# Kernel optimization log

Hardware: AMD Instinct MI355X
Metric: run time of the kernel (lower is better)

The kernel has to match this reference:

```python
import jax, jax.numpy as jnp
import numpy as np

N = 100000   # local subgraph nodes
E = 600000   # directed edges
D = 128      # memory_dim
B = 10000    # label nodes queried
C = 32       # num_classes


def _glorot(key, shape):
    s = 1.0 / np.sqrt(shape[0])
    return jax.random.uniform(key, shape, jnp.float32, -s, s)


def setup_inputs() -> dict:
    key = jax.random.key(0)
    ks = jax.random.split(key, 16)
    return {
        "node_state": jax.random.normal(ks[0], (N, D), jnp.float32),
        "edge_index": jax.random.randint(ks[1], (2, E), 0, N),
        "label_pos": jax.random.randint(ks[2], (B,), 0, N),
        # SAGEConv 1: lin_l (neighbor, with bias), lin_r (root, no bias)
        "W1l": _glorot(ks[3], (D, D)), "b1l": jnp.zeros((D,), jnp.float32),
        "W1r": _glorot(ks[4], (D, D)),
        # SAGEConv 2
        "W2l": _glorot(ks[5], (D, D)), "b2l": jnp.zeros((D,), jnp.float32),
        "W2r": _glorot(ks[6], (D, D)),
        # classifier: Linear(D,D) -> ReLU -> Linear(D,C)
        "Wc1": _glorot(ks[7], (D, D)), "bc1": jnp.zeros((D,), jnp.float32),
        "Wc2": _glorot(ks[8], (D, C)), "bc2": jnp.zeros((C,), jnp.float32),
    }


def _sage(x, src, dst, Wl, bl, Wr):
    # PyG SAGEConv, aggr='mean': out_i = lin_l(mean_{j: (j->i)} x_j) + lin_r(x_i)
    n = x.shape[0]
    agg = jax.ops.segment_sum(x[src], dst, num_segments=n)          # [N, D]
    cnt = jax.ops.segment_sum(jnp.ones_like(dst, x.dtype), dst, num_segments=n)
    mean = agg / jnp.maximum(cnt, 1.0)[:, None]
    return mean @ Wl + bl + x @ Wr


def reference(node_state, edge_index, label_pos,
              W1l, b1l, W1r, W2l, b2l, W2r, Wc1, bc1, Wc2, bc2):
    src, dst = edge_index[0], edge_index[1]
    x = jax.nn.relu(_sage(node_state, src, dst, W1l, b1l, W1r))
    x = jax.nn.relu(_sage(x, src, dst, W2l, b2l, W2r))
    h = jax.nn.relu(x[label_pos] @ Wc1 + bc1)                        # [B, D]
    return h @ Wc2 + bc2                                             # [B, C]
```

## Files before the change

### kernel.cpp

```cpp
#include <hip/hip_runtime.h>
#include <hip/hip_bf16.h>

static constexpr int N = 100000;
static constexpr int E = 600000;
static constexpr int D = 128;
static constexpr int B = 10000;
static constexpr int C = 32;
static constexpr int NB = (N + 1023) / 1024;
static constexpr int TOUCHB = (N * (D / 4) + 255) / 256;

typedef __attribute__((ext_vector_type(8))) short short8;
typedef __attribute__((ext_vector_type(4))) float f32x4;

static __device__ __forceinline__ unsigned short f2bf(float f) {
    unsigned u = __float_as_uint(f);
    unsigned r = (u + 0x7FFFu + ((u >> 16) & 1u)) >> 16;
    return (unsigned short)r;
}
static __device__ __forceinline__ float bf2f(unsigned short h) {
    return __uint_as_float(((unsigned)h) << 16);
}

static __device__ __forceinline__ void split8(const float4 v0, const float4 v1,
                                              short8& h, short8& l) {
    const float f[8] = {v0.x, v0.y, v0.z, v0.w, v1.x, v1.y, v1.z, v1.w};
    #pragma unroll
    for (int i = 0; i < 8; ++i) {
        unsigned short hh = f2bf(f[i]);
        h[i] = (short)hh;
        l[i] = (short)f2bf(f[i] - bf2f(hh));
    }
}

__global__ void lab_k(const int* __restrict__ label_pos, int* __restrict__ labflag,
                      int* __restrict__ flag, int nlab) {
    int i = blockIdx.x * blockDim.x + threadIdx.x;
    if (i < nlab) {
        int v = label_pos[i];
        labflag[v] = 1;
        flag[v] = 1;
    }
}

__global__ __launch_bounds__(256) void deg_swz_k(
    const int* __restrict__ src, const int* __restrict__ dst,
    const int* __restrict__ labflag,
    int* __restrict__ deg, int* __restrict__ flag, int nE, int EB,
    const float* W0, const float* W1, const float* W2, const float* W3,
    const float* W4, const float* W5,
    unsigned short* __restrict__ out,
    const float* __restrict__ xtouch, float* __restrict__ sink) {
    if ((int)blockIdx.x < EB) {
        int e = blockIdx.x * 256 + threadIdx.x;
        if (e < nE) {
            int d = dst[e];
            atomicAdd(&deg[d], 1);
            if (labflag[d]) flag[src[e]] = 1;
        }
        return;
    }
    if ((int)blockIdx.x < EB + 80) {
        const int sb = blockIdx.x - EB;
        const int m = sb >> 4;
        const int chunk = sb & 15;
        const float* W = (m == 0) ? W0 : (m == 1) ? W1 : (m == 2) ? W2
                       : (m == 3) ? W3 : W4;
        unsigned short* o = out + (size_t)m * 32768;
        #pragma unroll
        for (int it = 0; it < 4; ++it) {
            int f = chunk * 1024 + it * 256 + threadIdx.x;
            int j = f & 7;
            int lane = (f >> 3) & 63;
            int fi = f >> 9;
            int k = (fi >> 3) * 32 + (lane >> 4) * 8 + j;
            int n = (fi & 7) * 16 + (lane & 15);
            float a = W[k * 128 + n];
            unsigned short h = f2bf(a);
            o[f] = h;
            o[16384 + f] = f2bf(a - bf2f(h));
        }
        return;
    }
    if ((int)blockIdx.x == EB + 80) {
        unsigned short* o2 = out + (size_t)5 * 32768;
        #pragma unroll
        for (int it = 0; it < 16; ++it) {
            int f = it * 256 + threadIdx.x;
            int j = f & 7;
            int lane = (f >> 3) & 63;
            int fi = f >> 9;
            int k = (fi >> 1) * 32 + (lane >> 4) * 8 + j;
            int n = (fi & 1) * 16 + (lane & 15);
            float a = W5[k * 32 + n];
            unsigned short h = f2bf(a);
            o2[f] = h;
            o2[4096 + f] = f2bf(a - bf2f(h));
        }
        return;
    }
    const int f4 = (blockIdx.x - (EB + 81)) * 256 + threadIdx.x;
    if (f4 < N * (D / 4)) {
        float4 v = reinterpret_cast<const float4*>(xtouch)[f4];
        float s = v.x + v.y + v.z + v.w;
        if (s > 1e30f) *sink = s;
    }
}

__global__ __launch_bounds__(256) void scan1m_k(const int* __restrict__ deg,
                                                const int* __restrict__ flag,
                                                int* __restrict__ bsum, int n) {
    __shared__ int lsum[256];
    const int t = threadIdx.x;
    const bool isdeg = (int)blockIdx.x < NB;
    const int bloc = isdeg ? blockIdx.x : blockIdx.x - NB;
    const int* v = isdeg ? deg : flag;
    const int base = bloc * 1024 + t * 4;
    int s = 0;
    #pragma unroll
    for (int i = 0; i < 4; ++i) {
        int idx = base + i;
        if (idx < n) s += v[idx];
    }
    lsum[t] = s;
    __syncthreads();
    for (int off = 128; off > 0; off >>= 1) {
        if (t < off) lsum[t] += lsum[t + off];
        __syncthreads();
    }
    if (t == 0) bsum[blockIdx.x] = lsum[0];
}

__global__ __launch_bounds__(256) void scan3m_k(
    const int* __restrict__ deg, const int* __restrict__ flag,
    const int* __restrict__ bsum,
    int* __restrict__ roff, int* __restrict__ cur,
    int* __restrict__ map, int* __restrict__ ulist, int* __restrict__ ucnt,
    int n)
{
    __shared__ int sb[128];
    __shared__ int lsum[256];
    const int t = threadIdx.x;
    const bool isdeg = (int)blockIdx.x < NB;
    const int bloc = isdeg ? blockIdx.x : blockIdx.x - NB;
    const int* bs = isdeg ? bsum : bsum + NB;
    const int* v  = isdeg ? deg : flag;

    if (t < 128) sb[t] = (t < NB) ? bs[t] : 0;
    __syncthreads();
    for (int off = 1; off < 128; off <<= 1) {
        int u = (t < 128 && t >= off) ? sb[t - off] : 0;
        __syncthreads();
        if (t < 128) sb[t] += u;
        __syncthreads();
    }
    const int boff = (bloc == 0) ? 0 : sb[bloc - 1];
    if (bloc == 0 && t == 0) {
        if (isdeg) roff[n] = sb[NB - 1];
        else *ucnt = sb[NB - 1];
    }

    const int base = bloc * 1024 + t * 4;
    int d[4];
    int s = 0;
    #pragma unroll
    for (int i = 0; i < 4; ++i) {
        int idx = base + i;
        d[i] = (idx < n) ? v[idx] : 0;
        s += d[i];
    }
    lsum[t] = s;
    __syncthreads();
    for (int off = 1; off < 256; off <<= 1) {
        int u = (t >= off) ? lsum[t - off] : 0;
        __syncthreads();
        lsum[t] += u;
        __syncthreads();
    }
    int run = boff + lsum[t] - s;
    #pragma unroll
    for (int i = 0; i < 4; ++i) {
        int idx = base + i;
        if (idx < n) {
            if (isdeg) {
                roff[idx] = run;
                cur[idx]  = run;
                run += d[i];
            } else if (d[i]) {
                map[idx] = run;
                ulist[run] = idx;
                ++run;
            }
        }
    }
}

__global__ void fill_k(const int* __restrict__ src, const int* __restrict__ dst,
                       int* __restrict__ cur, int* __restrict__ csr_src, int nE) {
    int e = blockIdx.x * blockDim.x + threadIdx.x;
    if (e < nE) {
        int p = atomicAdd(&cur[dst[e]], 1);
        csr_src[p] = src[e];
    }
}

template <bool GATHER, bool MAP>
__global__ __launch_bounds__(256) void gather_mean_k(
    const float* __restrict__ x, const int* __restrict__ roff,
    const int* __restrict__ csr_src, const int* __restrict__ rows,
    const int* __restrict__ map, const int* __restrict__ nrows_ptr,
    float* __restrict__ out, int nrows_max) {
    const int nrows = nrows_ptr ? nrows_ptr[0] : nrows_max;
    const int w = blockIdx.x * (blockDim.x >> 6) + (threadIdx.x >> 6);
    if (w >= nrows) return;
    const int lane = threadIdx.x & 63;
    const int n  = GATHER ? rows[w] : w;
    const int jb = roff[n];
    const int je = roff[n + 1];
    const float* xb = x + lane * 2;

    float ax = 0.f, ay = 0.f;
    int j = jb;
    for (; j + 4 <= je; j += 4) {
        int s0 = csr_src[j + 0];
        int s1 = csr_src[j + 1];
        int s2 = csr_src[j + 2];
        int s3 = csr_src[j + 3];
        if (MAP) { s0 = map[s0]; s1 = map[s1]; s2 = map[s2]; s3 = map[s3]; }
        float2 v0 = *reinterpret_cast<const float2*>(xb + (size_t)s0 * D);
        float2 v1 = *reinterpret_cast<const float2*>(xb + (size_t)s1 * D);
        float2 v2 = *reinterpret_cast<const float2*>(xb + (size_t)s2 * D);
        float2 v3 = *reinterpret_cast<const float2*>(xb + (size_t)s3 * D);
        ax += v0.x + v1.x + v2.x + v3.x;
        ay += v0.y + v1.y + v2.y + v3.y;
    }
    for (; j < je; ++j) {
        int s = csr_src[j];
        if (MAP) s = map[s];
        float2 v = *reinterpret_cast<const float2*>(xb + (size_t)s * D);
        ax += v.x;
        ay += v.y;
    }
    const float inv = 1.0f / fmaxf((float)(je - jb), 1.0f);
    *reinterpret_cast<float2*>(out + (size_t)w * D + lane * 2) =
        make_float2(ax * inv, ay * inv);
}

template <bool GATHER, bool MAP>
__global__ __launch_bounds__(256, 6) void sage_mfma_k(
    const float* __restrict__ mean, const float* __restrict__ xsrc,
    const int* __restrict__ rows, const int* __restrict__ map,
    const int* __restrict__ nrows_ptr,
    const unsigned short* __restrict__ WlSw, const unsigned short* __restrict__ WrSw,
    const float* __restrict__ bl, float* __restrict__ xout, int nrows_max)
{
    const int nrows = nrows_ptr ? nrows_ptr[0] : nrows_max;
    const int rb = blockIdx.x * 32;
    if (rb >= nrows) return;

    const int t = threadIdx.x;
    const int wrow = (t >> 6) & 1;
    const int wcol = t >> 7;
    const int lane = t & 63;
    const int mcol = lane & 15;
    const int q = lane >> 4;
    const int r = rb + wrow * 16 + mcol;

    f32x4 acc[4];
    #pragma unroll
    for (int no = 0; no < 4; ++no) acc[no] = (f32x4){0.f, 0.f, 0.f, 0.f};

    size_t gidx = 0;
    if (r < nrows) {
        int g = GATHER ? rows[r] : r;
        if (MAP) g = map[g];
        gidx = (size_t)g;
    }

    #pragma unroll
    for (int br = 0; br < 2; ++br) {
        const unsigned short* __restrict__ Wm = br ? WrSw : WlSw;
        #pragma unroll
        for (int kp = 0; kp < 4; ++kp) {
            short8 aH, aL;
            {
                float4 v0 = make_float4(0.f, 0.f, 0.f, 0.f);
                float4 v1 = make_float4(0.f, 0.f, 0.f, 0.f);
                if (r < nrows) {
                    const float* p = (br == 0)
                        ? mean + (size_t)r * D + kp * 32 + q * 8
                        : xsrc + gidx * D + kp * 32 + q * 8;
                    v0 = *reinterpret_cast<const float4*>(p);
                    v1 = *reinterpret_cast<const float4*>(p + 4);
                }
                split8(v0, v1, aH, aL);
            }
            #pragma unroll
            for (int no = 0; no < 4; ++no) {
                const size_t fo = ((size_t)(kp * 8 + wcol * 4 + no) * 64 + lane) * 8;
                short8 bh = *reinterpret_cast<const short8*>(Wm + fo);
                short8 bo = *reinterpret_cast<const short8*>(Wm + 16384 + fo);
                acc[no] = __builtin_amdgcn_mfma_f32_16x16x32_bf16(aH, bh, acc[no], 0, 0, 0);
                acc[no] = __builtin_amdgcn_mfma_f32_16x16x32_bf16(aL, bh, acc[no], 0, 0, 0);
                acc[no] = __builtin_amdgcn_mfma_f32_16x16x32_bf16(aH, bo, acc[no], 0, 0, 0);
            }
        }
    }

    #pragma unroll
    for (int no = 0; no < 4; ++no) {
        const int col = wcol * 64 + no * 16 + mcol;
        const float bias = bl[col];
        #pragma unroll
        for (int ri = 0; ri < 4; ++ri) {
            const int row = rb + wrow * 16 + q * 4 + ri;
            if (row < nrows)
                xout[(size_t)row * D + col] = fmaxf(acc[no][ri] + bias, 0.f);
        }
    }
}

__global__ __launch_bounds__(256) void sage2_cls_k(
    const float* __restrict__ mean, const float* __restrict__ x1c,
    const int* __restrict__ label_pos, const int* __restrict__ map,
    const unsigned short* __restrict__ WlSw, const unsigned short* __restrict__ WrSw,
    const float* __restrict__ bl,
    const unsigned short* __restrict__ Wc1Sw, const float* __restrict__ bc1,
    const unsigned short* __restrict__ Wc2Sw, const float* __restrict__ bc2,
    float* __restrict__ out, int nrows)
{
    __shared__ alignas(16) float Xs[32][132];
    __shared__ alignas(16) float Hs[32][132];
    const int rb = blockIdx.x * 32;
    const int t = threadIdx.x;
    const int wrow = (t >> 6) & 1;
    const int wcol = t >> 7;
    const int lane = t & 63;
    const int mcol = lane & 15;
    const int q = lane >> 4;
    const int r = rb + wrow * 16 + mcol;

    f32x4 acc[4];
    #pragma unroll
    for (int no = 0; no < 4; ++no) acc[no] = (f32x4){0.f, 0.f, 0.f, 0.f};

    size_t gidx = 0;
    if (r < nrows) gidx = (size_t)map[label_pos[r]];

    #pragma unroll
    for (int br = 0; br < 2; ++br) {
        const unsigned short* __restrict__ Wm = br ? WrSw : WlSw;
        #pragma unroll
        for (int kp = 0; kp < 4; ++kp) {
            short8 aH, aL;
            {
                float4 v0 = make_float4(0.f, 0.f, 0.f, 0.f);
                float4 v1 = make_float4(0.f, 0.f, 0.f, 0.f);
                if (r < nrows) {
                    const float* p = (br == 0)
                        ? mean + (size_t)r * D + kp * 32 + q * 8
                        : x1c + gidx * D + kp * 32 + q * 8;
                    v0 = *reinterpret_cast<const float4*>(p);
                    v1 = *reinterpret_cast<const float4*>(p + 4);
                }
                split8(v0, v1, aH, aL);
            }
            #pragma unroll
            for (int no = 0; no < 4; ++no) {
                const size_t fo = ((size_t)(kp * 8 + wcol * 4 + no) * 64 + lane) * 8;
                short8 bh = *reinterpret_cast<const short8*>(Wm + fo);
                short8 bo = *reinterpret_cast<const short8*>(Wm + 16384 + fo);
                acc[no] = __builtin_amdgcn_mfma_f32_16x16x32_bf16(aH, bh, acc[no], 0, 0, 0);
                acc[no] = __builtin_amdgcn_mfma_f32_16x16x32_bf16(aL, bh, acc[no], 0, 0, 0);
                acc[no] = __builtin_amdgcn_mfma_f32_16x16x32_bf16(aH, bo, acc[no], 0, 0, 0);
            }
        }
    }

    #pragma unroll
    for (int no = 0; no < 4; ++no) {
        const int col = wcol * 64 + no * 16 + mcol;
        const float bias = bl[col];
        #pragma unroll
        for (int ri = 0; ri < 4; ++ri) {
            const int lrow = wrow * 16 + q * 4 + ri;
            Xs[lrow][col] = fmaxf(acc[no][ri] + bias, 0.f);
        }
    }
    __syncthreads();

    {
        f32x4 acc2[4];
        #pragma unroll
        for (int no = 0; no < 4; ++no) acc2[no] = (f32x4){0.f, 0.f, 0.f, 0.f};

        #pragma unroll
        for (int kp = 0; kp < 4; ++kp) {
            short8 aH, aL;
            {
                const float* p = &Xs[wrow * 16 + mcol][kp * 32 + q * 8];
                float4 v0 = *reinterpret_cast<const float4*>(p);
                float4 v1 = *reinterpret_cast<const float4*>(p + 4);
                split8(v0, v1, aH, aL);
            }
            #pragma unroll
            for (int no = 0; no < 4; ++no) {
                const size_t fo = ((size_t)(kp * 8 + wcol * 4 + no) * 64 + lane) * 8;
                short8 bh = *reinterpret_cast<const short8*>(Wc1Sw + fo);
                short8 bo = *reinterpret_cast<const short8*>(Wc1Sw + 16384 + fo);
                acc2[no] = __builtin_amdgcn_mfma_f32_16x16x32_bf16(aH, bh, acc2[no], 0, 0, 0);
                acc2[no] = __builtin_amdgcn_mfma_f32_16x16x32_bf16(aL, bh, acc2[no], 0, 0, 0);
                acc2[no] = __builtin_amdgcn_mfma_f32_16x16x32_bf16(aH, bo, acc2[no], 0, 0, 0);
            }
        }
        #pragma unroll
        for (int no = 0; no < 4; ++no) {
            const int col = wcol * 64 + no * 16 + mcol;
            const float bias = bc1[col];
            #pragma unroll
            for (int ri = 0; ri < 4; ++ri) {
                const int lrow = wrow * 16 + q * 4 + ri;
                Hs[lrow][col] = fmaxf(acc2[no][ri] + bias, 0.0f);
            }
        }
    }
    __syncthreads();

    {
        f32x4 acc3 = (f32x4){0.f, 0.f, 0.f, 0.f};
        #pragma unroll
        for (int kp = 0; kp < 4; ++kp) {
            short8 aH, aL;
            {
                const float* p = &Hs[wrow * 16 + mcol][kp * 32 + q * 8];
                float4 v0 = *reinterpret_cast<const float4*>(p);
                float4 v1 = *reinterpret_cast<const float4*>(p + 4);
                split8(v0, v1, aH, aL);
            }
            const size_t fo = ((size_t)(kp * 2 + wcol) * 64 + lane) * 8;
            short8 bh = *reinterpret_cast<const short8*>(Wc2Sw + fo);
            short8 bo = *reinterpret_cast<const short8*>(Wc2Sw + 4096 + fo);
            acc3 = __builtin_amdgcn_mfma_f32_16x16x32_bf16(aH, bh, acc3, 0, 0, 0);
            acc3 = __builtin_amdgcn_mfma_f32_16x16x32_bf16(aL, bh, acc3, 0, 0, 0);
            acc3 = __builtin_amdgcn_mfma_f32_16x16x32_bf16(aH, bo, acc3, 0, 0, 0);
        }
        const int col = wcol * 16 + mcol;
        const float b2 = bc2[col];
        #pragma unroll
        for (int ri = 0; ri < 4; ++ri) {
            const int row = rb + wrow * 16 + q * 4 + ri;
            if (row < nrows) out[(size_t)row * C + col] = acc3[ri] + b2;
        }
    }
}


extern "C" void kernel_launch(void* const* d_in, const int* in_sizes, int n_in,
                              void* d_out, int out_size, void* d_ws, size_t ws_size,
                              hipStream_t stream) {
    const float* node_state = (const float*)d_in[0];
    const int*   edge_index = (const int*)d_in[1];
    const int*   label_pos  = (const int*)d_in[2];
    const float* W1l = (const float*)d_in[3];
    const float* b1l = (const float*)d_in[4];
    const float* W1r = (const float*)d_in[5];
    const float* W2l = (const float*)d_in[6];
    const float* b2l = (const float*)d_in[7];
    const float* W2r = (const float*)d_in[8];
    const float* Wc1 = (const float*)d_in[9];
    const float* bc1 = (const float*)d_in[10];
    const float* Wc2 = (const float*)d_in[11];
    const float* bc2 = (const float*)d_in[12];
    float* out = (float*)d_out;

    const int* src = edge_index;
    const int* dst = edge_index + E;

    char* ws = (char*)d_ws;
    float* x1c   = (float*)ws;                    ws += sizeof(float) * (size_t)N * D;
    float* bufA  = (float*)ws;                    ws += sizeof(float) * (size_t)N * D;
    unsigned short* Wsw = (unsigned short*)ws;    ws += sizeof(unsigned short) * (5 * 32768 + 8192);
    int* deg     = (int*)ws;                      ws += sizeof(int) * N;
    int* flag    = (int*)ws;                      ws += sizeof(int) * N;
    int* labflag = (int*)ws;                      ws += sizeof(int) * N;
    int* ucnt    = (int*)ws;                      ws += sizeof(int);
    float* sink  = (float*)ws;                    ws += sizeof(float);
    ws += sizeof(int) * 2;
    int* roff    = (int*)ws;                      ws += sizeof(int) * (N + 1);
    int* cur     = (int*)ws;                      ws += sizeof(int) * N;
    int* csr_src = (int*)ws;                      ws += sizeof(int) * E;
    int* map     = (int*)ws;                      ws += sizeof(int) * N;
    int* ulist   = (int*)ws;                      ws += sizeof(int) * N;
    int* bsum    = (int*)ws;                      ws += sizeof(int) * 256;
    float* mean1c = bufA;
    float* mean2g = bufA;

    const int TB = 256;
    const int EB = (E + TB - 1) / TB;

    hipMemsetAsync(deg, 0, sizeof(int) * (3 * N + 1), stream);
    lab_k<<<(B + TB - 1) / TB, TB, 0, stream>>>(label_pos, labflag, flag, B);
    deg_swz_k<<<EB + 81 + TOUCHB, TB, 0, stream>>>(src, dst, labflag, deg, flag, E, EB,
                                                   W1l, W1r, W2l, W2r, Wc1, Wc2, Wsw,
                                                   node_state, sink);
    scan1m_k<<<2 * NB, 256, 0, stream>>>(deg, flag, bsum, N);
    scan3m_k<<<2 * NB, 256, 0, stream>>>(deg, flag, bsum, roff, cur, map, ulist, ucnt, N);
    fill_k<<<EB, TB, 0, stream>>>(src, dst, cur, csr_src, E);

    gather_mean_k<true, false><<<(N + 3) / 4, TB, 0, stream>>>(
        node_state, roff, csr_src, ulist, nullptr, ucnt, mean1c, N);
    sage_mfma_k<true, false><<<(N + 31) / 32, TB, 0, stream>>>(
        mean1c, node_state, ulist, nullptr, ucnt,
        Wsw, Wsw + 32768, b1l, x1c, N);

    gather_mean_k<true, true><<<(B + 3) / 4, TB, 0, stream>>>(
        x1c, roff, csr_src, label_pos, map, nullptr, mean2g, B);
    sage2_cls_k<<<(B + 31) / 32, TB, 0, stream>>>(
        mean2g, x1c, label_pos, map,
        Wsw + 65536, Wsw + 98304, b2l,
        Wsw + 131072, bc1,
        Wsw + 163840, bc2, out, B);
}
```

Measured before the change: 255.1 us.

## Fuse neighbor mean-gather into SAGE MFMA kernels and replace scans with atomic allocation

```diff
diff --git a/kernel.cpp b/kernel.cpp
--- a/kernel.cpp
+++ b/kernel.cpp
@@ -6,7 +6,6 @@
 static constexpr int D = 128;
 static constexpr int B = 10000;
 static constexpr int C = 32;
-static constexpr int NB = (N + 1023) / 1024;
 static constexpr int TOUCHB = (N * (D / 4) + 255) / 256;
 
 typedef __attribute__((ext_vector_type(8))) short short8;
@@ -106,161 +105,89 @@
     }
 }
 
-__global__ __launch_bounds__(256) void scan1m_k(const int* __restrict__ deg,
-                                                const int* __restrict__ flag,
-                                                int* __restrict__ bsum, int n) {
-    __shared__ int lsum[256];
-    const int t = threadIdx.x;
-    const bool isdeg = (int)blockIdx.x < NB;
-    const int bloc = isdeg ? blockIdx.x : blockIdx.x - NB;
-    const int* v = isdeg ? deg : flag;
-    const int base = bloc * 1024 + t * 4;
-    int s = 0;
-    #pragma unroll
-    for (int i = 0; i < 4; ++i) {
-        int idx = base + i;
-        if (idx < n) s += v[idx];
-    }
-    lsum[t] = s;
-    __syncthreads();
-    for (int off = 128; off > 0; off >>= 1) {
-        if (t < off) lsum[t] += lsum[t + off];
-        __syncthreads();
-    }
-    if (t == 0) bsum[blockIdx.x] = lsum[0];
-}
-
-__global__ __launch_bounds__(256) void scan3m_k(
+__global__ __launch_bounds__(256) void alloc_k(
     const int* __restrict__ deg, const int* __restrict__ flag,
-    const int* __restrict__ bsum,
     int* __restrict__ roff, int* __restrict__ cur,
-    int* __restrict__ map, int* __restrict__ ulist, int* __restrict__ ucnt,
-    int n)
+    int* __restrict__ map, int* __restrict__ ulist,
+    int* __restrict__ ucnt, int* __restrict__ total, int n)
 {
-    __shared__ int sb[128];
-    __shared__ int lsum[256];
-    const int t = threadIdx.x;
-    const bool isdeg = (int)blockIdx.x < NB;
-    const int bloc = isdeg ? blockIdx.x : blockIdx.x - NB;
-    const int* bs = isdeg ? bsum : bsum + NB;
-    const int* v  = isdeg ? deg : flag;
-
-    if (t < 128) sb[t] = (t < NB) ? bs[t] : 0;
-    __syncthreads();
-    for (int off = 1; off < 128; off <<= 1) {
-        int u = (t < 128 && t >= off) ? sb[t - off] : 0;
-        __syncthreads();
-        if (t < 128) sb[t] += u;
-        __syncthreads();
-    }
-    const int boff = (bloc == 0) ? 0 : sb[bloc - 1];
-    if (bloc == 0 && t == 0) {
-        if (isdeg) roff[n] = sb[NB - 1];
-        else *ucnt = sb[NB - 1];
-    }
-
-    const int base = bloc * 1024 + t * 4;
-    int d[4];
-    int s = 0;
-    #pragma unroll
-    for (int i = 0; i < 4; ++i) {
-        int idx = base + i;
-        d[i] = (idx < n) ? v[idx] : 0;
-        s += d[i];
-    }
-    lsum[t] = s;
-    __syncthreads();
-    for (int off = 1; off < 256; off <<= 1) {
-        int u = (t >= off) ? lsum[t - off] : 0;
-        __syncthreads();
-        lsum[t] += u;
-        __syncthreads();
-    }
-    int run = boff + lsum[t] - s;
-    #pragma unroll
-    for (int i = 0; i < 4; ++i) {
-        int idx = base + i;
-        if (idx < n) {
-            if (isdeg) {
-                roff[idx] = run;
-                cur[idx]  = run;
-                run += d[i];
-            } else if (d[i]) {
-                map[idx] = run;
-                ulist[run] = idx;
-                ++run;
-            }
-        }
+    int i = blockIdx.x * 256 + threadIdx.x;
+    if (i < n && flag[i]) {
+        int m = atomicAdd(ucnt, 1);
+        map[i] = m;
+        ulist[m] = i;
+        int d = deg[i];
+        int p = atomicAdd(total, d);
+        roff[i] = p;
+        cur[i] = p;
     }
 }
 
 __global__ void fill_k(const int* __restrict__ src, const int* __restrict__ dst,
+                       const int* __restrict__ flag,
                        int* __restrict__ cur, int* __restrict__ csr_src, int nE) {
     int e = blockIdx.x * blockDim.x + threadIdx.x;
     if (e < nE) {
-        int p = atomicAdd(&cur[dst[e]], 1);
-        csr_src[p] = src[e];
-    }
-}
-
-template <bool GATHER, bool MAP>
-__global__ __launch_bounds__(256) void gather_mean_k(
+        int d = dst[e];
+        if (flag[d]) {
+            int p = atomicAdd(&cur[d], 1);
+            csr_src[p] = src[e];
+        }
+    }
+}
+
+__global__ __launch_bounds__(256, 6) void sage1_fused_k(
     const float* __restrict__ x, const int* __restrict__ roff,
-    const int* __restrict__ csr_src, const int* __restrict__ rows,
-    const int* __restrict__ map, const int* __restrict__ nrows_ptr,
-    float* __restrict__ out, int nrows_max) {
-    const int nrows = nrows_ptr ? nrows_ptr[0] : nrows_max;
-    const int w = blockIdx.x * (blockDim.x >> 6) + (threadIdx.x >> 6);
-    if (w >= nrows) return;
-    const int lane = threadIdx.x & 63;
-    const int n  = GATHER ? rows[w] : w;
-    const int jb = roff[n];
-    const int je = roff[n + 1];
-    const float* xb = x + lane * 2;
-
-    float ax = 0.f, ay = 0.f;
-    int j = jb;
-    for (; j + 4 <= je; j += 4) {
-        int s0 = csr_src[j + 0];
-        int s1 = csr_src[j + 1];
-        int s2 = csr_src[j + 2];
-        int s3 = csr_src[j + 3];
-        if (MAP) { s0 = map[s0]; s1 = map[s1]; s2 = map[s2]; s3 = map[s3]; }
-        float2 v0 = *reinterpret_cast<const float2*>(xb + (size_t)s0 * D);
-        float2 v1 = *reinterpret_cast<const float2*>(xb + (size_t)s1 * D);
-        float2 v2 = *reinterpret_cast<const float2*>(xb + (size_t)s2 * D);
-        float2 v3 = *reinterpret_cast<const float2*>(xb + (size_t)s3 * D);
-        ax += v0.x + v1.x + v2.x + v3.x;
-        ay += v0.y + v1.y + v2.y + v3.y;
-    }
-    for (; j < je; ++j) {
-        int s = csr_src[j];
-        if (MAP) s = map[s];
-        float2 v = *reinterpret_cast<const float2*>(xb + (size_t)s * D);
-        ax += v.x;
-        ay += v.y;
-    }
-    const float inv = 1.0f / fmaxf((float)(je - jb), 1.0f);
-    *reinterpret_cast<float2*>(out + (size_t)w * D + lane * 2) =
-        make_float2(ax * inv, ay * inv);
-}
-
-template <bool GATHER, bool MAP>
-__global__ __launch_bounds__(256, 6) void sage_mfma_k(
-    const float* __restrict__ mean, const float* __restrict__ xsrc,
-    const int* __restrict__ rows, const int* __restrict__ map,
-    const int* __restrict__ nrows_ptr,
+    const int* __restrict__ deg, const int* __restrict__ csr_src,
+    const int* __restrict__ ulist, const int* __restrict__ nrows_ptr,
     const unsigned short* __restrict__ WlSw, const unsigned short* __restrict__ WrSw,
-    const float* __restrict__ bl, float* __restrict__ xout, int nrows_max)
+    const float* __restrict__ bl, float* __restrict__ xout)
 {
-    const int nrows = nrows_ptr ? nrows_ptr[0] : nrows_max;
+    __shared__ alignas(16) float Ms[32][132];
+    const int nrows = nrows_ptr[0];
     const int rb = blockIdx.x * 32;
     if (rb >= nrows) return;
 
     const int t = threadIdx.x;
-    const int wrow = (t >> 6) & 1;
-    const int wcol = t >> 7;
     const int lane = t & 63;
+    const int w = t >> 6;
+
+    {
+        const float* xb = x + lane * 2;
+        for (int lr8 = 0; lr8 < 8; ++lr8) {
+            const int lr = w * 8 + lr8;
+            const int r = rb + lr;
+            int jb = 0, je = 0;
+            if (r < nrows) { const int n = ulist[r]; jb = roff[n]; je = jb + deg[n]; }
+            float ax = 0.f, ay = 0.f;
+            int j = jb;
+            for (; j + 4 <= je; j += 4) {
+                const int s0 = csr_src[j + 0];
+                const int s1 = csr_src[j + 1];
+                const int s2 = csr_src[j + 2];
+                const int s3 = csr_src[j + 3];
+                float2 v0 = *reinterpret_cast<const float2*>(xb + (size_t)s0 * D);
+                float2 v1 = *reinterpret_cast<const float2*>(xb + (size_t)s1 * D);
+                float2 v2 = *reinterpret_cast<const float2*>(xb + (size_t)s2 * D);
+                float2 v3 = *reinterpret_cast<const float2*>(xb + (size_t)s3 * D);
+                ax += v0.x + v1.x + v2.x + v3.x;
+                ay += v0.y + v1.y + v2.y + v3.y;
+            }
+            for (; j < je; ++j) {
+                const int s = csr_src[j];
+                float2 v = *reinterpret_cast<const float2*>(xb + (size_t)s * D);
+                ax += v.x;
+                ay += v.y;
+            }
+            const float inv = 1.0f / fmaxf((float)(je - jb), 1.0f);
+            Ms[lr][lane * 2]     = ax * inv;
+            Ms[lr][lane * 2 + 1] = ay * inv;
+        }
+    }
+    __syncthreads();
+
+    const int wrow = w & 1;
+    const int wcol = w >> 1;
     const int mcol = lane & 15;
     const int q = lane >> 4;
     const int r = rb + wrow * 16 + mcol;
@@ -270,11 +197,7 @@
     for (int no = 0; no < 4; ++no) acc[no] = (f32x4){0.f, 0.f, 0.f, 0.f};
 
     size_t gidx = 0;
-    if (r < nrows) {
-        int g = GATHER ? rows[r] : r;
-        if (MAP) g = map[g];
-        gidx = (size_t)g;
-    }
+    if (r < nrows) gidx = (size_t)ulist[r];
 
     #pragma unroll
     for (int br = 0; br < 2; ++br) {
@@ -283,14 +206,19 @@
         for (int kp = 0; kp < 4; ++kp) {
             short8 aH, aL;
             {
-                float4 v0 = make_float4(0.f, 0.f, 0.f, 0.f);
-                float4 v1 = make_float4(0.f, 0.f, 0.f, 0.f);
-                if (r < nrows) {
-                    const float* p = (br == 0)
-                        ? mean + (size_t)r * D + kp * 32 + q * 8
-                        : xsrc + gidx * D + kp * 32 + q * 8;
+                float4 v0, v1;
+                if (br == 0) {
+                    const float* p = &Ms[wrow * 16 + mcol][kp * 32 + q * 8];
                     v0 = *reinterpret_cast<const float4*>(p);
                     v1 = *reinterpret_cast<const float4*>(p + 4);
+                } else {
+                    v0 = make_float4(0.f, 0.f, 0.f, 0.f);
+                    v1 = make_float4(0.f, 0.f, 0.f, 0.f);
+                    if (r < nrows) {
+                        const float* p = x + gidx * D + kp * 32 + q * 8;
+                        v0 = *reinterpret_cast<const float4*>(p);
+                        v1 = *reinterpret_cast<const float4*>(p + 4);
+                    }
                 }
                 split8(v0, v1, aH, aL);
             }
@@ -319,8 +247,9 @@
     }
 }
 
-__global__ __launch_bounds__(256) void sage2_cls_k(
-    const float* __restrict__ mean, const float* __restrict__ x1c,
+__global__ __launch_bounds__(256) void sage2_cls_fused_k(
+    const float* __restrict__ x1c, const int* __restrict__ roff,
+    const int* __restrict__ deg, const int* __restrict__ csr_src,
     const int* __restrict__ label_pos, const int* __restrict__ map,
     const unsigned short* __restrict__ WlSw, const unsigned short* __restrict__ WrSw,
     const float* __restrict__ bl,
@@ -328,13 +257,50 @@
     const unsigned short* __restrict__ Wc2Sw, const float* __restrict__ bc2,
     float* __restrict__ out, int nrows)
 {
+    __shared__ alignas(16) float Ms[32][132];
     __shared__ alignas(16) float Xs[32][132];
     __shared__ alignas(16) float Hs[32][132];
     const int rb = blockIdx.x * 32;
     const int t = threadIdx.x;
-    const int wrow = (t >> 6) & 1;
-    const int wcol = t >> 7;
     const int lane = t & 63;
+    const int w = t >> 6;
+
+    {
+        const float* xb = x1c + lane * 2;
+        for (int lr8 = 0; lr8 < 8; ++lr8) {
+            const int lr = w * 8 + lr8;
+            const int r = rb + lr;
+            int jb = 0, je = 0;
+            if (r < nrows) { const int n = label_pos[r]; jb = roff[n]; je = jb + deg[n]; }
+            float ax = 0.f, ay = 0.f;
+            int j = jb;
+            for (; j + 4 <= je; j += 4) {
+                const int s0 = map[csr_src[j + 0]];
+                const int s1 = map[csr_src[j + 1]];
+                const int s2 = map[csr_src[j + 2]];
+                const int s3 = map[csr_src[j + 3]];
+                float2 v0 = *reinterpret_cast<const float2*>(xb + (size_t)s0 * D);
+                float2 v1 = *reinterpret_cast<const float2*>(xb + (size_t)s1 * D);
+                float2 v2 = *reinterpret_cast<const float2*>(xb + (size_t)s2 * D);
+                float2 v3 = *reinterpret_cast<const float2*>(xb + (size_t)s3 * D);
+                ax += v0.x + v1.x + v2.x + v3.x;
+                ay += v0.y + v1.y + v2.y + v3.y;
+            }
+            for (; j < je; ++j) {
+                const int s = map[csr_src[j]];
+                float2 v = *reinterpret_cast<const float2*>(xb + (size_t)s * D);
+                ax += v.x;
+                ay += v.y;
+            }
+            const float inv = 1.0f / fmaxf((float)(je - jb), 1.0f);
+            Ms[lr][lane * 2]     = ax * inv;
+            Ms[lr][lane * 2 + 1] = ay * inv;
+        }
+    }
+    __syncthreads();
+
+    const int wrow = w & 1;
+    const int wcol = w >> 1;
     const int mcol = lane & 15;
     const int q = lane >> 4;
     const int r = rb + wrow * 16 + mcol;
@@ -353,14 +319,19 @@
         for (int kp = 0; kp < 4; ++kp) {
             short8 aH, aL;
             {
-                float4 v0 = make_float4(0.f, 0.f, 0.f, 0.f);
-                float4 v1 = make_float4(0.f, 0.f, 0.f, 0.f);
-                if (r < nrows) {
-                    const float* p = (br == 0)
-                        ? mean + (size_t)r * D + kp * 32 + q * 8
-                        : x1c + gidx * D + kp * 32 + q * 8;
+                float4 v0, v1;
+                if (br == 0) {
+                    const float* p = &Ms[wrow * 16 + mcol][kp * 32 + q * 8];
                     v0 = *reinterpret_cast<const float4*>(p);
                     v1 = *reinterpret_cast<const float4*>(p + 4);
+                } else {
+                    v0 = make_float4(0.f, 0.f, 0.f, 0.f);
+                    v1 = make_float4(0.f, 0.f, 0.f, 0.f);
+                    if (r < nrows) {
+                        const float* p = x1c + gidx * D + kp * 32 + q * 8;
+                        v0 = *reinterpret_cast<const float4*>(p);
+                        v1 = *reinterpret_cast<const float4*>(p + 4);
+                    }
                 }
                 split8(v0, v1, aH, aL);
             }
@@ -477,45 +448,38 @@
 
     char* ws = (char*)d_ws;
     float* x1c   = (float*)ws;                    ws += sizeof(float) * (size_t)N * D;
-    float* bufA  = (float*)ws;                    ws += sizeof(float) * (size_t)N * D;
     unsigned short* Wsw = (unsigned short*)ws;    ws += sizeof(unsigned short) * (5 * 32768 + 8192);
     int* deg     = (int*)ws;                      ws += sizeof(int) * N;
     int* flag    = (int*)ws;                      ws += sizeof(int) * N;
     int* labflag = (int*)ws;                      ws += sizeof(int) * N;
     int* ucnt    = (int*)ws;                      ws += sizeof(int);
+    int* total   = (int*)ws;                      ws += sizeof(int);
     float* sink  = (float*)ws;                    ws += sizeof(float);
-    ws += sizeof(int) * 2;
-    int* roff    = (int*)ws;                      ws += sizeof(int) * (N + 1);
+    ws += sizeof(int);
+    int* roff    = (int*)ws;                      ws += sizeof(int) * N;
     int* cur     = (int*)ws;                      ws += sizeof(int) * N;
     int* csr_src = (int*)ws;                      ws += sizeof(int) * E;
     int* map     = (int*)ws;                      ws += sizeof(int) * N;
     int* ulist   = (int*)ws;                      ws += sizeof(int) * N;
-    int* bsum    = (int*)ws;                      ws += sizeof(int) * 256;
-    float* mean1c = bufA;
-    float* mean2g = bufA;
 
     const int TB = 256;
     const int EB = (E + TB - 1) / TB;
 
-    hipMemsetAsync(deg, 0, sizeof(int) * (3 * N + 1), stream);
+    hipMemsetAsync(deg, 0, sizeof(int) * (3 * N + 2), stream);
     lab_k<<<(B + TB - 1) / TB, TB, 0, stream>>>(label_pos, labflag, flag, B);
     deg_swz_k<<<EB + 81 + TOUCHB, TB, 0, stream>>>(src, dst, labflag, deg, flag, E, EB,
                                                    W1l, W1r, W2l, W2r, Wc1, Wc2, Wsw,
                                                    node_state, sink);
-    scan1m_k<<<2 * NB, 256, 0, stream>>>(deg, flag, bsum, N);
-    scan3m_k<<<2 * NB, 256, 0, stream>>>(deg, flag, bsum, roff, cur, map, ulist, ucnt, N);
-    fill_k<<<EB, TB, 0, stream>>>(src, dst, cur, csr_src, E);
-
-    gather_mean_k<true, false><<<(N + 3) / 4, TB, 0, stream>>>(
-        node_state, roff, csr_src, ulist, nullptr, ucnt, mean1c, N);
-    sage_mfma_k<true, false><<<(N + 31) / 32, TB, 0, stream>>>(
-        mean1c, node_state, ulist, nullptr, ucnt,
-        Wsw, Wsw + 32768, b1l, x1c, N);
-
-    gather_mean_k<true, true><<<(B + 3) / 4, TB, 0, stream>>>(
-        x1c, roff, csr_src, label_pos, map, nullptr, mean2g, B);
-    sage2_cls_k<<<(B + 31) / 32, TB, 0, stream>>>(
-        mean2g, x1c, label_pos, map,
+    alloc_k<<<(N + TB - 1) / TB, TB, 0, stream>>>(deg, flag, roff, cur, map, ulist,
+                                                  ucnt, total, N);
+    fill_k<<<EB, TB, 0, stream>>>(src, dst, flag, cur, csr_src, E);
+
+    sage1_fused_k<<<(N + 31) / 32, TB, 0, stream>>>(
+        node_state, roff, deg, csr_src, ulist, ucnt,
+        Wsw, Wsw + 32768, b1l, x1c);
+
+    sage2_cls_fused_k<<<(B + 31) / 32, TB, 0, stream>>>(
+        x1c, roff, deg, csr_src, label_pos, map,
         Wsw + 65536, Wsw + 98304, b2l,
         Wsw + 131072, bc1,
         Wsw + 163840, bc2, out, B);
```

Result: slower. 278.0 us (+9.0%).

## Replace two-pass scan with atomic allocation and build CSR only for needed nodes

Applied to the files above, without the earlier changes.

```diff
diff --git a/kernel.cpp b/kernel.cpp
--- a/kernel.cpp
+++ b/kernel.cpp
@@ -6,7 +6,6 @@
 static constexpr int D = 128;
 static constexpr int B = 10000;
 static constexpr int C = 32;
-static constexpr int NB = (N + 1023) / 1024;
 static constexpr int TOUCHB = (N * (D / 4) + 255) / 256;
 
 typedef __attribute__((ext_vector_type(8))) short short8;
@@ -106,108 +105,43 @@
     }
 }
 
-__global__ __launch_bounds__(256) void scan1m_k(const int* __restrict__ deg,
-                                                const int* __restrict__ flag,
-                                                int* __restrict__ bsum, int n) {
-    __shared__ int lsum[256];
-    const int t = threadIdx.x;
-    const bool isdeg = (int)blockIdx.x < NB;
-    const int bloc = isdeg ? blockIdx.x : blockIdx.x - NB;
-    const int* v = isdeg ? deg : flag;
-    const int base = bloc * 1024 + t * 4;
-    int s = 0;
-    #pragma unroll
-    for (int i = 0; i < 4; ++i) {
-        int idx = base + i;
-        if (idx < n) s += v[idx];
-    }
-    lsum[t] = s;
-    __syncthreads();
-    for (int off = 128; off > 0; off >>= 1) {
-        if (t < off) lsum[t] += lsum[t + off];
-        __syncthreads();
-    }
-    if (t == 0) bsum[blockIdx.x] = lsum[0];
-}
-
-__global__ __launch_bounds__(256) void scan3m_k(
+__global__ __launch_bounds__(256) void alloc_k(
     const int* __restrict__ deg, const int* __restrict__ flag,
-    const int* __restrict__ bsum,
     int* __restrict__ roff, int* __restrict__ cur,
-    int* __restrict__ map, int* __restrict__ ulist, int* __restrict__ ucnt,
-    int n)
+    int* __restrict__ map, int* __restrict__ ulist,
+    int* __restrict__ ucnt, int* __restrict__ total, int n)
 {
-    __shared__ int sb[128];
-    __shared__ int lsum[256];
-    const int t = threadIdx.x;
-    const bool isdeg = (int)blockIdx.x < NB;
-    const int bloc = isdeg ? blockIdx.x : blockIdx.x - NB;
-    const int* bs = isdeg ? bsum : bsum + NB;
-    const int* v  = isdeg ? deg : flag;
-
-    if (t < 128) sb[t] = (t < NB) ? bs[t] : 0;
-    __syncthreads();
-    for (int off = 1; off < 128; off <<= 1) {
-        int u = (t < 128 && t >= off) ? sb[t - off] : 0;
-        __syncthreads();
-        if (t < 128) sb[t] += u;
-        __syncthreads();
-    }
-    const int boff = (bloc == 0) ? 0 : sb[bloc - 1];
-    if (bloc == 0 && t == 0) {
-        if (isdeg) roff[n] = sb[NB - 1];
-        else *ucnt = sb[NB - 1];
-    }
-
-    const int base = bloc * 1024 + t * 4;
-    int d[4];
-    int s = 0;
-    #pragma unroll
-    for (int i = 0; i < 4; ++i) {
-        int idx = base + i;
-        d[i] = (idx < n) ? v[idx] : 0;
-        s += d[i];
-    }
-    lsum[t] = s;
-    __syncthreads();
-    for (int off = 1; off < 256; off <<= 1) {
-        int u = (t >= off) ? lsum[t - off] : 0;
-        __syncthreads();
-        lsum[t] += u;
-        __syncthreads();
-    }
-    int run = boff + lsum[t] - s;
-    #pragma unroll
-    for (int i = 0; i < 4; ++i) {
-        int idx = base + i;
-        if (idx < n) {
-            if (isdeg) {
-                roff[idx] = run;
-                cur[idx]  = run;
-                run += d[i];
-            } else if (d[i]) {
-                map[idx] = run;
-                ulist[run] = idx;
-                ++run;
-            }
-        }
+    int i = blockIdx.x * 256 + threadIdx.x;
+    if (i < n && flag[i]) {
+        int m = atomicAdd(ucnt, 1);
+        map[i] = m;
+        ulist[m] = i;
+        int d = deg[i];
+        int p = atomicAdd(total, d);
+        roff[i] = p;
+        cur[i] = p;
     }
 }
 
 __global__ void fill_k(const int* __restrict__ src, const int* __restrict__ dst,
+                       const int* __restrict__ flag,
                        int* __restrict__ cur, int* __restrict__ csr_src, int nE) {
     int e = blockIdx.x * blockDim.x + threadIdx.x;
     if (e < nE) {
-        int p = atomicAdd(&cur[dst[e]], 1);
-        csr_src[p] = src[e];
+        int d = dst[e];
+        if (flag[d]) {
+            int p = atomicAdd(&cur[d], 1);
+            csr_src[p] = src[e];
+        }
     }
 }
 
 template <bool GATHER, bool MAP>
 __global__ __launch_bounds__(256) void gather_mean_k(
     const float* __restrict__ x, const int* __restrict__ roff,
-    const int* __restrict__ csr_src, const int* __restrict__ rows,
-    const int* __restrict__ map, const int* __restrict__ nrows_ptr,
+    const int* __restrict__ deg, const int* __restrict__ csr_src,
+    const int* __restrict__ rows, const int* __restrict__ map,
+    const int* __restrict__ nrows_ptr,
     float* __restrict__ out, int nrows_max) {
     const int nrows = nrows_ptr ? nrows_ptr[0] : nrows_max;
     const int w = blockIdx.x * (blockDim.x >> 6) + (threadIdx.x >> 6);
@@ -215,32 +149,26 @@
     const int lane = threadIdx.x & 63;
     const int n  = GATHER ? rows[w] : w;
     const int jb = roff[n];
-    const int je = roff[n + 1];
+    const int dg = deg[n];
+    const int je = jb + dg;
     const float* xb = x + lane * 2;
 
     float ax = 0.f, ay = 0.f;
-    int j = jb;
-    for (; j + 4 <= je; j += 4) {
-        int s0 = csr_src[j + 0];
-        int s1 = csr_src[j + 1];
-        int s2 = csr_src[j + 2];
-        int s3 = csr_src[j + 3];
-        if (MAP) { s0 = map[s0]; s1 = map[s1]; s2 = map[s2]; s3 = map[s3]; }
-        float2 v0 = *reinterpret_cast<const float2*>(xb + (size_t)s0 * D);
-        float2 v1 = *reinterpret_cast<const float2*>(xb + (size_t)s1 * D);
-        float2 v2 = *reinterpret_cast<const float2*>(xb + (size_t)s2 * D);
-        float2 v3 = *reinterpret_cast<const float2*>(xb + (size_t)s3 * D);
-        ax += v0.x + v1.x + v2.x + v3.x;
-        ay += v0.y + v1.y + v2.y + v3.y;
-    }
-    for (; j < je; ++j) {
-        int s = csr_src[j];
-        if (MAP) s = map[s];
-        float2 v = *reinterpret_cast<const float2*>(xb + (size_t)s * D);
-        ax += v.x;
-        ay += v.y;
-    }
-    const float inv = 1.0f / fmaxf((float)(je - jb), 1.0f);
+    for (int j = jb; j < je; j += 8) {
+        float2 vv[8];
+        #pragma unroll
+        for (int u = 0; u < 8; ++u) {
+            const int jj = j + u;
+            int s = csr_src[(jj < je) ? jj : jb];
+            if (MAP) s = map[s];
+            vv[u] = *reinterpret_cast<const float2*>(xb + (size_t)s * D);
+        }
+        #pragma unroll
+        for (int u = 0; u < 8; ++u) {
+            if (j + u < je) { ax += vv[u].x; ay += vv[u].y; }
+        }
+    }
+    const float inv = 1.0f / fmaxf((float)dg, 1.0f);
     *reinterpret_cast<float2*>(out + (size_t)w * D + lane * 2) =
         make_float2(ax * inv, ay * inv);
 }
@@ -483,37 +411,37 @@
     int* flag    = (int*)ws;                      ws += sizeof(int) * N;
     int* labflag = (int*)ws;                      ws += sizeof(int) * N;
     int* ucnt    = (int*)ws;                      ws += sizeof(int);
+    int* total   = (int*)ws;                      ws += sizeof(int);
     float* sink  = (float*)ws;                    ws += sizeof(float);
-    ws += sizeof(int) * 2;
-    int* roff    = (int*)ws;                      ws += sizeof(int) * (N + 1);
+    ws += sizeof(int);
+    int* roff    = (int*)ws;                      ws += sizeof(int) * N;
     int* cur     = (int*)ws;                      ws += sizeof(int) * N;
     int* csr_src = (int*)ws;                      ws += sizeof(int) * E;
     int* map     = (int*)ws;                      ws += sizeof(int) * N;
     int* ulist   = (int*)ws;                      ws += sizeof(int) * N;
-    int* bsum    = (int*)ws;                      ws += sizeof(int) * 256;
     float* mean1c = bufA;
     float* mean2g = bufA;
 
     const int TB = 256;
     const int EB = (E + TB - 1) / TB;
 
-    hipMemsetAsync(deg, 0, sizeof(int) * (3 * N + 1), stream);
+    hipMemsetAsync(deg, 0, sizeof(int) * (3 * N + 2), stream);
     lab_k<<<(B + TB - 1) / TB, TB, 0, stream>>>(label_pos, labflag, flag, B);
     deg_swz_k<<<EB + 81 + TOUCHB, TB, 0, stream>>>(src, dst, labflag, deg, flag, E, EB,
                                                    W1l, W1r, W2l, W2r, Wc1, Wc2, Wsw,
                                                    node_state, sink);
-    scan1m_k<<<2 * NB, 256, 0, stream>>>(deg, flag, bsum, N);
-    scan3m_k<<<2 * NB, 256, 0, stream>>>(deg, flag, bsum, roff, cur, map, ulist, ucnt, N);
-    fill_k<<<EB, TB, 0, stream>>>(src, dst, cur, csr_src, E);
+    alloc_k<<<(N + TB - 1) / TB, TB, 0, stream>>>(deg, flag, roff, cur, map, ulist,
+                                                  ucnt, total, N);
+    fill_k<<<EB, TB, 0, stream>>>(src, dst, flag, cur, csr_src, E);
 
     gather_mean_k<true, false><<<(N + 3) / 4, TB, 0, stream>>>(
-        node_state, roff, csr_src, ulist, nullptr, ucnt, mean1c, N);
+        node_state, roff, deg, csr_src, ulist, nullptr, ucnt, mean1c, N);
     sage_mfma_k<true, false><<<(N + 31) / 32, TB, 0, stream>>>(
         mean1c, node_state, ulist, nullptr, ucnt,
         Wsw, Wsw + 32768, b1l, x1c, N);
 
     gather_mean_k<true, true><<<(B + 3) / 4, TB, 0, stream>>>(
-        x1c, roff, csr_src, label_pos, map, nullptr, mean2g, B);
+        x1c, roff, deg, csr_src, label_pos, map, nullptr, mean2g, B);
     sage2_cls_k<<<(B + 31) / 32, TB, 0, stream>>>(
         mean2g, x1c, label_pos, map,
         Wsw + 65536, Wsw + 98304, b2l,
```

Measured after the change: 276.0 us. 1.08x slower.

## Replace CSR build and gather with atomic scatter-add aggregation

Applied to the files above, without the earlier changes.

```diff
diff --git a/kernel.cpp b/kernel.cpp
--- a/kernel.cpp
+++ b/kernel.cpp
@@ -33,23 +33,25 @@
 }
 
 __global__ void lab_k(const int* __restrict__ label_pos, int* __restrict__ labflag,
-                      int* __restrict__ flag, int nlab) {
+                      int* __restrict__ flag, int* __restrict__ labrank, int nlab) {
     int i = blockIdx.x * blockDim.x + threadIdx.x;
     if (i < nlab) {
         int v = label_pos[i];
         labflag[v] = 1;
         flag[v] = 1;
-    }
-}
-
-__global__ __launch_bounds__(256) void deg_swz_k(
+        labrank[v] = i;
+    }
+}
+
+__global__ __launch_bounds__(256) void pass1_k(
     const int* __restrict__ src, const int* __restrict__ dst,
     const int* __restrict__ labflag,
     int* __restrict__ deg, int* __restrict__ flag, int nE, int EB,
     const float* W0, const float* W1, const float* W2, const float* W3,
     const float* W4, const float* W5,
     unsigned short* __restrict__ out,
-    const float* __restrict__ xtouch, float* __restrict__ sink) {
+    const float* __restrict__ xtouch, float* __restrict__ agg1,
+    float* __restrict__ sink) {
     if ((int)blockIdx.x < EB) {
         int e = blockIdx.x * 256 + threadIdx.x;
         if (e < nE) {
@@ -101,25 +103,22 @@
     const int f4 = (blockIdx.x - (EB + 81)) * 256 + threadIdx.x;
     if (f4 < N * (D / 4)) {
         float4 v = reinterpret_cast<const float4*>(xtouch)[f4];
+        reinterpret_cast<float4*>(agg1)[f4] = make_float4(0.f, 0.f, 0.f, 0.f);
         float s = v.x + v.y + v.z + v.w;
         if (s > 1e30f) *sink = s;
     }
 }
 
-__global__ __launch_bounds__(256) void scan1m_k(const int* __restrict__ deg,
-                                                const int* __restrict__ flag,
+__global__ __launch_bounds__(256) void scan1f_k(const int* __restrict__ flag,
                                                 int* __restrict__ bsum, int n) {
     __shared__ int lsum[256];
     const int t = threadIdx.x;
-    const bool isdeg = (int)blockIdx.x < NB;
-    const int bloc = isdeg ? blockIdx.x : blockIdx.x - NB;
-    const int* v = isdeg ? deg : flag;
-    const int base = bloc * 1024 + t * 4;
+    const int base = blockIdx.x * 1024 + t * 4;
     int s = 0;
     #pragma unroll
     for (int i = 0; i < 4; ++i) {
         int idx = base + i;
-        if (idx < n) s += v[idx];
+        if (idx < n) s += flag[idx];
     }
     lsum[t] = s;
     __syncthreads();
@@ -130,22 +129,15 @@
     if (t == 0) bsum[blockIdx.x] = lsum[0];
 }
 
-__global__ __launch_bounds__(256) void scan3m_k(
-    const int* __restrict__ deg, const int* __restrict__ flag,
-    const int* __restrict__ bsum,
-    int* __restrict__ roff, int* __restrict__ cur,
-    int* __restrict__ map, int* __restrict__ ulist, int* __restrict__ ucnt,
-    int n)
+__global__ __launch_bounds__(256) void scan3f_k(
+    const int* __restrict__ flag, const int* __restrict__ bsum,
+    int* __restrict__ map, int* __restrict__ ulist, int* __restrict__ ucnt, int n)
 {
     __shared__ int sb[128];
     __shared__ int lsum[256];
     const int t = threadIdx.x;
-    const bool isdeg = (int)blockIdx.x < NB;
-    const int bloc = isdeg ? blockIdx.x : blockIdx.x - NB;
-    const int* bs = isdeg ? bsum : bsum + NB;
-    const int* v  = isdeg ? deg : flag;
-
-    if (t < 128) sb[t] = (t < NB) ? bs[t] : 0;
+
+    if (t < 128) sb[t] = (t < NB) ? bsum[t] : 0;
     __syncthreads();
     for (int off = 1; off < 128; off <<= 1) {
         int u = (t < 128 && t >= off) ? sb[t - off] : 0;
@@ -153,19 +145,16 @@
         if (t < 128) sb[t] += u;
         __syncthreads();
     }
-    const int boff = (bloc == 0) ? 0 : sb[bloc - 1];
-    if (bloc == 0 && t == 0) {
-        if (isdeg) roff[n] = sb[NB - 1];
-        else *ucnt = sb[NB - 1];
-    }
-
-    const int base = bloc * 1024 + t * 4;
+    const int boff = (blockIdx.x == 0) ? 0 : sb[blockIdx.x - 1];
+    if (blockIdx.x == 0 && t == 0) *ucnt = sb[NB - 1];
+
+    const int base = blockIdx.x * 1024 + t * 4;
     int d[4];
     int s = 0;
     #pragma unroll
     for (int i = 0; i < 4; ++i) {
         int idx = base + i;
-        d[i] = (idx < n) ? v[idx] : 0;
+        d[i] = (idx < n) ? flag[idx] : 0;
         s += d[i];
     }
     lsum[t] = s;
@@ -180,80 +169,58 @@
     #pragma unroll
     for (int i = 0; i < 4; ++i) {
         int idx = base + i;
-        if (idx < n) {
-            if (isdeg) {
-                roff[idx] = run;
-                cur[idx]  = run;
-                run += d[i];
-            } else if (d[i]) {
-                map[idx] = run;
-                ulist[run] = idx;
-                ++run;
-            }
-        }
-    }
-}
-
-__global__ void fill_k(const int* __restrict__ src, const int* __restrict__ dst,
-                       int* __restrict__ cur, int* __restrict__ csr_src, int nE) {
-    int e = blockIdx.x * blockDim.x + threadIdx.x;
-    if (e < nE) {
-        int p = atomicAdd(&cur[dst[e]], 1);
-        csr_src[p] = src[e];
-    }
-}
-
-template <bool GATHER, bool MAP>
-__global__ __launch_bounds__(256) void gather_mean_k(
-    const float* __restrict__ x, const int* __restrict__ roff,
-    const int* __restrict__ csr_src, const int* __restrict__ rows,
-    const int* __restrict__ map, const int* __restrict__ nrows_ptr,
-    float* __restrict__ out, int nrows_max) {
-    const int nrows = nrows_ptr ? nrows_ptr[0] : nrows_max;
-    const int w = blockIdx.x * (blockDim.x >> 6) + (threadIdx.x >> 6);
-    if (w >= nrows) return;
+        if (idx < n && d[i]) {
+            map[idx] = run;
+            ulist[run] = idx;
+            ++run;
+        }
+    }
+}
+
+__global__ __launch_bounds__(256) void scatter1_k(
+    const int* __restrict__ src, const int* __restrict__ dst,
+    const int* __restrict__ flag,
+    const float* __restrict__ x, float* __restrict__ agg1, int nE)
+{
+    const int w = blockIdx.x * 4 + (threadIdx.x >> 6);
+    if (w >= nE) return;
+    const int d = dst[w];
+    if (!flag[d]) return;
+    const int s = src[w];
     const int lane = threadIdx.x & 63;
-    const int n  = GATHER ? rows[w] : w;
-    const int jb = roff[n];
-    const int je = roff[n + 1];
-    const float* xb = x + lane * 2;
-
-    float ax = 0.f, ay = 0.f;
-    int j = jb;
-    for (; j + 4 <= je; j += 4) {
-        int s0 = csr_src[j + 0];
-        int s1 = csr_src[j + 1];
-        int s2 = csr_src[j + 2];
-        int s3 = csr_src[j + 3];
-        if (MAP) { s0 = map[s0]; s1 = map[s1]; s2 = map[s2]; s3 = map[s3]; }
-        float2 v0 = *reinterpret_cast<const float2*>(xb + (size_t)s0 * D);
-        float2 v1 = *reinterpret_cast<const float2*>(xb + (size_t)s1 * D);
-        float2 v2 = *reinterpret_cast<const float2*>(xb + (size_t)s2 * D);
-        float2 v3 = *reinterpret_cast<const float2*>(xb + (size_t)s3 * D);
-        ax += v0.x + v1.x + v2.x + v3.x;
-        ay += v0.y + v1.y + v2.y + v3.y;
-    }
-    for (; j < je; ++j) {
-        int s = csr_src[j];
-        if (MAP) s = map[s];
-        float2 v = *reinterpret_cast<const float2*>(xb + (size_t)s * D);
-        ax += v.x;
-        ay += v.y;
-    }
-    const float inv = 1.0f / fmaxf((float)(je - jb), 1.0f);
-    *reinterpret_cast<float2*>(out + (size_t)w * D + lane * 2) =
-        make_float2(ax * inv, ay * inv);
-}
-
-template <bool GATHER, bool MAP>
+    float2 v = *reinterpret_cast<const float2*>(x + (size_t)s * D + lane * 2);
+    float* a = agg1 + (size_t)d * D + lane * 2;
+    atomicAdd(a, v.x);
+    atomicAdd(a + 1, v.y);
+}
+
+__global__ __launch_bounds__(256) void scatter2_k(
+    const int* __restrict__ src, const int* __restrict__ dst,
+    const int* __restrict__ labflag, const int* __restrict__ labrank,
+    const int* __restrict__ map,
+    const float* __restrict__ x1c, float* __restrict__ agg2, int nE)
+{
+    const int w = blockIdx.x * 4 + (threadIdx.x >> 6);
+    if (w >= nE) return;
+    const int d = dst[w];
+    if (!labflag[d]) return;
+    const int s = map[src[w]];
+    const int lr = labrank[d];
+    const int lane = threadIdx.x & 63;
+    float2 v = *reinterpret_cast<const float2*>(x1c + (size_t)s * D + lane * 2);
+    float* a = agg2 + (size_t)lr * D + lane * 2;
+    atomicAdd(a, v.x);
+    atomicAdd(a + 1, v.y);
+}
+
 __global__ __launch_bounds__(256, 6) void sage_mfma_k(
-    const float* __restrict__ mean, const float* __restrict__ xsrc,
-    const int* __restrict__ rows, const int* __restrict__ map,
+    const float* __restrict__ agg1, const int* __restrict__ deg,
+    const float* __restrict__ xsrc, const int* __restrict__ ulist,
     const int* __restrict__ nrows_ptr,
     const unsigned short* __restrict__ WlSw, const unsigned short* __restrict__ WrSw,
-    const float* __restrict__ bl, float* __restrict__ xout, int nrows_max)
+    const float* __restrict__ bl, float* __restrict__ xout)
 {
-    const int nrows = nrows_ptr ? nrows_ptr[0] : nrows_max;
+    const int nrows = nrows_ptr[0];
     const int rb = blockIdx.x * 32;
     if (rb >= nrows) return;
 
@@ -270,10 +237,11 @@
     for (int no = 0; no < 4; ++no) acc[no] = (f32x4){0.f, 0.f, 0.f, 0.f};
 
     size_t gidx = 0;
+    float invd = 0.f;
     if (r < nrows) {
-        int g = GATHER ? rows[r] : r;
-        if (MAP) g = map[g];
+        int g = ulist[r];
         gidx = (size_t)g;
+        invd = 1.0f / fmaxf((float)deg[g], 1.0f);
     }
 
     #pragma unroll
@@ -287,10 +255,14 @@
                 float4 v1 = make_float4(0.f, 0.f, 0.f, 0.f);
                 if (r < nrows) {
                     const float* p = (br == 0)
-                        ? mean + (size_t)r * D + kp * 32 + q * 8
+                        ? agg1 + gidx * D + kp * 32 + q * 8
                         : xsrc + gidx * D + kp * 32 + q * 8;
                     v0 = *reinterpret_cast<const float4*>(p);
                     v1 = *reinterpret_cast<const float4*>(p + 4);
+                    if (br == 0) {
+                        v0.x *= invd; v0.y *= invd; v0.z *= invd; v0.w *= invd;
+                        v1.x *= invd; v1.y *= invd; v1.z *= invd; v1.w *= invd;
+                    }
                 }
                 split8(v0, v1, aH, aL);
             }
@@ -320,8 +292,10 @@
 }
 
 __global__ __launch_bounds__(256) void sage2_cls_k(
-    const float* __restrict__ mean, const float* __restrict__ x1c,
+    const float* __restrict__ agg2, const int* __restrict__ deg,
+    const float* __restrict__ x1c,
     const int* __restrict__ label_pos, const int* __restrict__ map,
+    const int* __restrict__ labrank,
     const unsigned short* __restrict__ WlSw, const unsigned short* __restrict__ WrSw,
     const float* __restrict__ bl,
     const unsigned short* __restrict__ Wc1Sw, const float* __restrict__ bc1,
@@ -343,8 +317,14 @@
     #pragma unroll
     for (int no = 0; no < 4; ++no) acc[no] = (f32x4){0.f, 0.f, 0.f, 0.f};
 
-    size_t gidx = 0;
-    if (r < nrows) gidx = (size_t)map[label_pos[r]];
+    size_t gidx = 0, aidx = 0;
+    float invd = 0.f;
+    if (r < nrows) {
+        const int n = label_pos[r];
+        gidx = (size_t)map[n];
+        aidx = (size_t)labrank[n];
+        invd = 1.0f / fmaxf((float)deg[n], 1.0f);
+    }
 
     #pragma unroll
     for (int br = 0; br < 2; ++br) {
@@ -357,10 +337,14 @@
                 float4 v1 = make_float4(0.f, 0.f, 0.f, 0.f);
                 if (r < nrows) {
                     const float* p = (br == 0)
-                        ? mean + (size_t)r * D + kp * 32 + q * 8
+                        ? agg2 + aidx * D + kp * 32 + q * 8
                         : x1c + gidx * D + kp * 32 + q * 8;
                     v0 = *reinterpret_cast<const float4*>(p);
                     v1 = *reinterpret_cast<const float4*>(p + 4);
+                    if (br == 0) {
+                        v0.x *= invd; v0.y *= invd; v0.z *= invd; v0.w *= invd;
+                        v1.x *= invd; v1.y *= invd; v1.z *= invd; v1.w *= invd;
+                    }
                 }
                 split8(v0, v1, aH, aL);
             }
@@ -477,7 +461,8 @@
 
     char* ws = (char*)d_ws;
     float* x1c   = (float*)ws;                    ws += sizeof(float) * (size_t)N * D;
-    float* bufA  = (float*)ws;                    ws += sizeof(float) * (size_t)N * D;
+    float* agg1  = (float*)ws;                    ws += sizeof(float) * (size_t)N * D;
+    float* agg2  = (float*)ws;                    ws += sizeof(float) * (size_t)B * D;
     unsigned short* Wsw = (unsigned short*)ws;    ws += sizeof(unsigned short) * (5 * 32768 + 8192);
     int* deg     = (int*)ws;                      ws += sizeof(int) * N;
     int* flag    = (int*)ws;                      ws += sizeof(int) * N;
@@ -485,37 +470,32 @@
     int* ucnt    = (int*)ws;                      ws += sizeof(int);
     float* sink  = (float*)ws;                    ws += sizeof(float);
     ws += sizeof(int) * 2;
-    int* roff    = (int*)ws;                      ws += sizeof(int) * (N + 1);
-    int* cur     = (int*)ws;                      ws += sizeof(int) * N;
-    int* csr_src = (int*)ws;                      ws += sizeof(int) * E;
+    int* labrank = (int*)ws;                      ws += sizeof(int) * N;
     int* map     = (int*)ws;                      ws += sizeof(int) * N;
     int* ulist   = (int*)ws;                      ws += sizeof(int) * N;
-    int* bsum    = (int*)ws;                      ws += sizeof(int) * 256;
-    float* mean1c = bufA;
-    float* mean2g = bufA;
+    int* bsum    = (int*)ws;                      ws += sizeof(int) * 128;
 
     const int TB = 256;
     const int EB = (E + TB - 1) / TB;
+    const int SB = (E + 3) / 4;
 
     hipMemsetAsync(deg, 0, sizeof(int) * (3 * N + 1), stream);
-    lab_k<<<(B + TB - 1) / TB, TB, 0, stream>>>(label_pos, labflag, flag, B);
-    deg_swz_k<<<EB + 81 + TOUCHB, TB, 0, stream>>>(src, dst, labflag, deg, flag, E, EB,
-                                                   W1l, W1r, W2l, W2r, Wc1, Wc2, Wsw,
-                                                   node_state, sink);
-    scan1m_k<<<2 * NB, 256, 0, stream>>>(deg, flag, bsum, N);
-    scan3m_k<<<2 * NB, 256, 0, stream>>>(deg, flag, bsum, roff, cur, map, ulist, ucnt, N);
-    fill_k<<<EB, TB, 0, stream>>>(src, dst, cur, csr_src, E);
-
-    gather_mean_k<true, false><<<(N + 3) / 4, TB, 0, stream>>>(
-        node_state, roff, csr_src, ulist, nullptr, ucnt, mean1c, N);
-    sage_mfma_k<true, false><<<(N + 31) / 32, TB, 0, stream>>>(
-        mean1c, node_state, ulist, nullptr, ucnt,
-        Wsw, Wsw + 32768, b1l, x1c, N);
-
-    gather_mean_k<true, true><<<(B + 3) / 4, TB, 0, stream>>>(
-        x1c, roff, csr_src, label_pos, map, nullptr, mean2g, B);
+    hipMemsetAsync(agg2, 0, sizeof(float) * (size_t)B * D, stream);
+    lab_k<<<(B + TB - 1) / TB, TB, 0, stream>>>(label_pos, labflag, flag, labrank, B);
+    pass1_k<<<EB + 81 + TOUCHB, TB, 0, stream>>>(src, dst, labflag, deg, flag, E, EB,
+                                                 W1l, W1r, W2l, W2r, Wc1, Wc2, Wsw,
+                                                 node_state, agg1, sink);
+    scan1f_k<<<NB, 256, 0, stream>>>(flag, bsum, N);
+    scan3f_k<<<NB, 256, 0, stream>>>(flag, bsum, map, ulist, ucnt, N);
+
+    scatter1_k<<<SB, TB, 0, stream>>>(src, dst, flag, node_state, agg1, E);
+    sage_mfma_k<<<(N + 31) / 32, TB, 0, stream>>>(
+        agg1, deg, node_state, ulist, ucnt,
+        Wsw, Wsw + 32768, b1l, x1c);
+
+    scatter2_k<<<SB, TB, 0, stream>>>(src, dst, labflag, labrank, map, x1c, agg2, E);
     sage2_cls_k<<<(B + 31) / 32, TB, 0, stream>>>(
-        mean2g, x1c, label_pos, map,
+        agg2, deg, x1c, label_pos, map, labrank,
         Wsw + 65536, Wsw + 98304, b2l,
         Wsw + 131072, bc1,
         Wsw + 163840, bc2, out, B);
```

After: 521.6 us. 104% more time.
